# Kernel optimization log

Hardware: AMD Instinct MI355X
Metric: run time of the kernel (lower is better)

The kernel has to match this reference:

```python
import jax, jax.numpy as jnp
import numpy as np

N_EXPERTS = 8
D_MODEL = 1024
D_FF = 4096
TOP_K = 2
B, S = 1, 2048


def setup_inputs() -> dict:
    key = jax.random.key(0)
    ks = jax.random.split(key, 5)
    scale_in = 1.0 / np.sqrt(D_MODEL)
    scale_ff = 1.0 / np.sqrt(D_FF)
    return {
        "x": jax.random.normal(ks[0], (B, S, D_MODEL), dtype=jnp.float32),
        "w_gate": jax.random.normal(ks[1], (D_MODEL, N_EXPERTS), dtype=jnp.float32) * scale_in,
        "b_gate": jnp.zeros((N_EXPERTS,), dtype=jnp.float32),
        "w1": jax.random.normal(ks[2], (N_EXPERTS, D_MODEL, D_FF), dtype=jnp.float32) * scale_in,
        "b1": jnp.zeros((N_EXPERTS, D_FF), dtype=jnp.float32),
        "w2": jax.random.normal(ks[3], (N_EXPERTS, D_FF, D_MODEL), dtype=jnp.float32) * scale_ff,
        "b2": jnp.zeros((N_EXPERTS, D_MODEL), dtype=jnp.float32),
    }


def reference(x, w_gate, b_gate, w1, b1, w2, b2):
    d = x.shape[-1]
    xs = x.reshape(-1, d)                       # [T, d]
    T = xs.shape[0]

    # --- routing: top-k gate logits, softmax over the k selected slots ---
    gate_logits = xs @ w_gate + b_gate          # [T, E]
    topk_vals, topk_idx = jax.lax.top_k(gate_logits, TOP_K)   # [T, k]
    weights = jax.nn.softmax(topk_vals, axis=-1)              # [T, k]

    # scatter slot weights into a dense [T, E] combine matrix
    comb = jnp.zeros((T, N_EXPERTS), dtype=xs.dtype)
    comb = comb.at[jnp.arange(T)[:, None], topk_idx].add(weights)

    # --- expert FFNs computed densely, combined with routing weights ---
    h = jax.nn.relu(jnp.einsum('td,edf->etf', xs, w1) + b1[:, None, :])  # [E, T, ff]
    y = jnp.einsum('etf,efd->etd', h, w2) + b2[:, None, :]               # [E, T, d]
    out = jnp.einsum('te,etd->td', comb, y)                              # [T, d]
    return out.reshape(x.shape)
```

## Files before the change

### kernel.cpp

```cpp
#include <hip/hip_runtime.h>
#include <hip/hip_bf16.h>
#include <math.h>

#define T_TOK 2048
#define DM    1024
#define DF    4096
#define NE    8
#define BM    128
#define BN    128
#define BK    64
#define LDA2  72
#define LDAV1 40
#define YROWS 5120

typedef __attribute__((ext_vector_type(8))) short          bf16x8;
typedef __attribute__((ext_vector_type(8))) unsigned short ushort8;
typedef __attribute__((ext_vector_type(4))) float          f32x4;

__device__ __forceinline__ unsigned short f2bf(float f) {
  unsigned u = __builtin_bit_cast(unsigned, f);
  unsigned r = u + 0x7fffu + ((u >> 16) & 1u);
  return (unsigned short)(r >> 16);
}

__global__ void convert_x_kernel(const float* __restrict__ x, unsigned short* __restrict__ xb) {
  int i = blockIdx.x * blockDim.x + threadIdx.x;
  const float* src = x + (size_t)i * 8;
  float4 a = *(const float4*)(src);
  float4 b = *(const float4*)(src + 4);
  ushort8 v;
  v[0] = f2bf(a.x); v[1] = f2bf(a.y); v[2] = f2bf(a.z); v[3] = f2bf(a.w);
  v[4] = f2bf(b.x); v[5] = f2bf(b.y); v[6] = f2bf(b.z); v[7] = f2bf(b.w);
  *(ushort8*)(xb + (size_t)i * 8) = v;
}

template<int K, int N>
__global__ __launch_bounds__(256) void transpose_convert_packed(
    const float* __restrict__ W, unsigned short* __restrict__ Wt)
{
  const int e  = blockIdx.z;
  const int kt = blockIdx.y;
  const int nt = blockIdx.x;
  const int k0 = kt * 64;
  const int n0 = nt * 128;
  const float* Wp = W + (size_t)e * K * N;
  __shared__ float Ls[64][129];
  const int tid = threadIdx.x;
  {
    const int kl = tid >> 5;
    const int nl = (tid & 31) * 4;
#pragma unroll
    for (int p = 0; p < 8; p++) {
      const int k = kl + p * 8;
      float4 v = *(const float4*)(Wp + (size_t)(k0 + k) * N + n0 + nl);
      Ls[k][nl + 0] = v.x; Ls[k][nl + 1] = v.y; Ls[k][nl + 2] = v.z; Ls[k][nl + 3] = v.w;
    }
  }
  __syncthreads();
  unsigned short* Wo = Wt + ((((size_t)e * (N / 128) + nt) * (K / 64) + kt) * 128) * 64;
  {
    const int n  = tid & 127;
    const int c0 = tid >> 7;
#pragma unroll
    for (int p = 0; p < 4; p++) {
      const int c = c0 + p * 2;
      ushort8 o;
#pragma unroll
      for (int j = 0; j < 8; j++) o[j] = f2bf(Ls[c * 8 + j][n]);
      *(ushort8*)(Wo + (size_t)n * 64 + c * 8) = o;
    }
  }
}

__global__ __launch_bounds__(256) void gating_kernel(
    const float* __restrict__ x, const float* __restrict__ wg, const float* __restrict__ bg,
    int* __restrict__ cnt, int* __restrict__ perm, float* __restrict__ pw,
    int* __restrict__ tok2slot, float* __restrict__ tokw)
{
  int wid  = (blockIdx.x * blockDim.x + threadIdx.x) >> 6;
  int lane = threadIdx.x & 63;
  if (wid >= T_TOK) return;
  const float* xr = x + (size_t)wid * DM;

  float acc[NE];
#pragma unroll
  for (int e = 0; e < NE; e++) acc[e] = 0.f;

  for (int d = lane; d < DM; d += 64) {
    float xv = xr[d];
    const float* wr = wg + (size_t)d * NE;
#pragma unroll
    for (int e = 0; e < NE; e++) acc[e] += xv * wr[e];
  }
#pragma unroll
  for (int off = 32; off > 0; off >>= 1) {
#pragma unroll
    for (int e = 0; e < NE; e++) acc[e] += __shfl_xor(acc[e], off, 64);
  }
  if (lane == 0) {
    float v[NE];
#pragma unroll
    for (int e = 0; e < NE; e++) v[e] = acc[e] + bg[e];
    int i0 = 0; float v0 = v[0];
#pragma unroll
    for (int e = 1; e < NE; e++) { if (v[e] > v0) { v0 = v[e]; i0 = e; } }
    int i1 = -1; float v1 = -INFINITY;
#pragma unroll
    for (int e = 0; e < NE; e++) { if (e != i0 && v[e] > v1) { v1 = v[e]; i1 = e; } }
    float e1 = expf(v1 - v0);
    float s  = 1.f + e1;
    float w0 = 1.f / s, w1 = e1 / s;
    int p0 = atomicAdd(&cnt[i0], 1);
    perm[i0 * T_TOK + p0] = wid; pw[i0 * T_TOK + p0] = w0;
    int p1 = atomicAdd(&cnt[i1], 1);
    perm[i1 * T_TOK + p1] = wid; pw[i1 * T_TOK + p1] = w1;
    tok2slot[2 * wid + 0] = (i0 << 16) | p0;  tokw[2 * wid + 0] = w0;
    tok2slot[2 * wid + 1] = (i1 << 16) | p1;  tokw[2 * wid + 1] = w1;
  }
}

__global__ void pad_scan_kernel(const int* __restrict__ cnt, int* __restrict__ cntpad,
                                int* __restrict__ offs, int* __restrict__ perm, float* __restrict__ pw)
{
  if (threadIdx.x == 0) {
    int o = 0;
    for (int e = 0; e < NE; e++) {
      int c  = cnt[e];
      int cp = (c + BM - 1) / BM * BM;
      cntpad[e] = cp;
      offs[e]   = o;
      o += cp;
    }
    offs[NE] = o;
  }
  for (int e = 0; e < NE; e++) {
    int c  = cnt[e];
    int cp = (c + BM - 1) / BM * BM;
    for (int i = c + threadIdx.x; i < cp; i += blockDim.x) {
      perm[e * T_TOK + i] = 0;
      pw[e * T_TOK + i]   = 0.f;
    }
  }
}

__global__ __launch_bounds__(256) void combine_kernel(
    const float* __restrict__ y0, const float* __restrict__ y1,
    const int* __restrict__ offs, const int* __restrict__ tok2slot,
    const float* __restrict__ tokw, float* __restrict__ out)
{
  const int t = blockIdx.x;
  const int d = threadIdx.x * 4;
  const int s0 = tok2slot[2 * t + 0];
  const int s1 = tok2slot[2 * t + 1];
  const float w0 = tokw[2 * t + 0];
  const float w1 = tokw[2 * t + 1];
  const size_t r0 = (size_t)(offs[s0 >> 16] + (s0 & 0xffff)) * DM + d;
  const size_t r1 = (size_t)(offs[s1 >> 16] + (s1 & 0xffff)) * DM + d;
  float4 a0 = *(const float4*)(y0 + r0);
  float4 b0 = *(const float4*)(y1 + r0);
  float4 a1 = *(const float4*)(y0 + r1);
  float4 b1 = *(const float4*)(y1 + r1);
  float4 o;
  o.x = w0 * (a0.x + b0.x) + w1 * (a1.x + b1.x);
  o.y = w0 * (a0.y + b0.y) + w1 * (a1.y + b1.y);
  o.z = w0 * (a0.z + b0.z) + w1 * (a1.z + b1.z);
  o.w = w0 * (a0.w + b0.w) + w1 * (a1.w + b1.w);
  *(float4*)(out + (size_t)t * DM + d) = o;
}

template<int PHASE, int KTOT, int NCOLS, int KSPLIT>
__global__ __launch_bounds__(256, 3) void moe_gemm5(
    const unsigned short* __restrict__ Asrc,
    const unsigned short* __restrict__ Bt,
    const float* __restrict__ bias,
    const int* __restrict__ cntpad, const int* __restrict__ offs,
    const int* __restrict__ perm,
    unsigned short* __restrict__ Hout, float* __restrict__ yout)
{
  const int e  = blockIdx.z;
  const int mt = blockIdx.y;
  const int nt = blockIdx.x / KSPLIT;
  const int ks = blockIdx.x % KSPLIT;
  const int cp = cntpad[e];
  if (mt * BM >= cp) return;
  const int tid = threadIdx.x;
  const int oe  = offs[e];

  __shared__ unsigned short As[BM * LDA2];
  __shared__ unsigned short Bs[BN * LDA2];

  const int am = tid >> 1;
  const int ak = (tid & 1) * 32;
  const int kb0 = ks * (KTOT / KSPLIT);
  const int KITERS = (KTOT / KSPLIT) / BK;

  const unsigned short* Ap;
  size_t APITCH;
  if (PHASE == 1) {
    int token = perm[e * T_TOK + mt * BM + am];
    Ap = Asrc + (size_t)token * KTOT + kb0 + ak;
    APITCH = BK;
  } else {
    const size_t rb = (size_t)(oe >> 7) + mt;
    Ap = Asrc + (((rb * (KTOT / 64) + (kb0 >> 6)) * 128 + am) * 64) + ak;
    APITCH = (size_t)128 * 64;
  }
  const unsigned short* Bp =
      Bt + ((((size_t)e * (NCOLS / 128) + nt) * (KTOT / 64) + (kb0 >> 6)) * 128 + am) * 64 + ak;

  const int wid  = tid >> 6;
  const int lane = tid & 63;
  const int wm   = (wid & 1) * 64;
  const int wn   = (wid >> 1) * 64;
  const int lrow = lane & 15;
  const int lk   = (lane >> 4) * 8;

  f32x4 acc[4][4];
#pragma unroll
  for (int i = 0; i < 4; i++)
#pragma unroll
    for (int j = 0; j < 4; j++) acc[i][j] = (f32x4){0.f, 0.f, 0.f, 0.f};

  uint4 pa0, pa1, pa2, pa3, pb0, pb1, pb2, pb3;
  auto LOADT = [&](int kt) {
    const unsigned short* a = Ap + (size_t)kt * APITCH;
    const unsigned short* b = Bp + (size_t)kt * (128 * 64);
    pa0 = *(const uint4*)(a);      pa1 = *(const uint4*)(a + 8);
    pa2 = *(const uint4*)(a + 16); pa3 = *(const uint4*)(a + 24);
    pb0 = *(const uint4*)(b);      pb1 = *(const uint4*)(b + 8);
    pb2 = *(const uint4*)(b + 16); pb3 = *(const uint4*)(b + 24);
  };
  auto STORET = [&]() {
    unsigned short* as = &As[am * LDA2 + ak];
    unsigned short* bs = &Bs[am * LDA2 + ak];
    *(uint4*)(as)      = pa0; *(uint4*)(as + 8)  = pa1;
    *(uint4*)(as + 16) = pa2; *(uint4*)(as + 24) = pa3;
    *(uint4*)(bs)      = pb0; *(uint4*)(bs + 8)  = pb1;
    *(uint4*)(bs + 16) = pb2; *(uint4*)(bs + 24) = pb3;
  };

  LOADT(0);
  STORET();
  for (int kt = 0; kt < KITERS; kt++) {
    __syncthreads();
    if (kt + 1 < KITERS) LOADT(kt + 1);
#pragma unroll
    for (int ksb = 0; ksb < 2; ksb++) {
      bf16x8 af[4], bfr[4];
#pragma unroll
      for (int i = 0; i < 4; i++)
        af[i]  = *(const bf16x8*)&As[(wm + i * 16 + lrow) * LDA2 + ksb * 32 + lk];
#pragma unroll
      for (int j = 0; j < 4; j++)
        bfr[j] = *(const bf16x8*)&Bs[(wn + j * 16 + lrow) * LDA2 + ksb * 32 + lk];
#pragma unroll
      for (int i = 0; i < 4; i++)
#pragma unroll
        for (int j = 0; j < 4; j++)
          acc[i][j] = __builtin_amdgcn_mfma_f32_16x16x32_bf16(af[i], bfr[j], acc[i][j], 0, 0, 0);
    }
    __syncthreads();
    if (kt + 1 < KITERS) STORET();
  }

  const int crow = (lane >> 4) * 4;
  const int ccol = lane & 15;
  const size_t rbh = (size_t)(oe >> 7) + mt;
  float* yp = yout + (size_t)ks * ((size_t)YROWS * NCOLS);
#pragma unroll
  for (int j = 0; j < 4; j++) {
    const int gn = nt * BN + wn + j * 16 + ccol;
    const float bv = bias[e * NCOLS + gn];
#pragma unroll
    for (int i = 0; i < 4; i++) {
#pragma unroll
      for (int r = 0; r < 4; r++) {
        const int lm = wm + i * 16 + crow + r;
        float v = acc[i][j][r];
        if (PHASE == 1) {
          v += bv;
          v = v > 0.f ? v : 0.f;
          Hout[(((rbh * (NCOLS / 64) + (gn >> 6)) * 128 + lm) * 64) + (gn & 63)] = f2bf(v);
        } else {
          if (ks == 0) v += bv;
          yp[(size_t)(oe + mt * BM + lm) * NCOLS + gn] = v;
        }
      }
    }
  }
}

template<int PHASE, int KTOT, int NCOLS, int KSPLIT>
__global__ __launch_bounds__(256) void moe_gemm_v1(
    const unsigned short* __restrict__ Asrc,
    const float* __restrict__ Wbase,
    const float* __restrict__ bias,
    const int* __restrict__ cntpad, const int* __restrict__ offs,
    const int* __restrict__ perm, const float* __restrict__ pw,
    unsigned short* __restrict__ Hout, float* __restrict__ out)
{
  const int e  = blockIdx.z;
  const int mt = blockIdx.y;
  const int nt = blockIdx.x / KSPLIT;
  const int ks = blockIdx.x % KSPLIT;
  const int cp = cntpad[e];
  if (mt * BM >= cp) return;
  const int tid = threadIdx.x;
  const int oe  = offs[e];

  __shared__ unsigned short As[BM * LDAV1];
  __shared__ unsigned short Bs[BN * LDAV1];

  const int am = tid >> 1;
  const int ak = (tid & 1) * 16;
  size_t arow_off;
  if (PHASE == 1) {
    int token = perm[e * T_TOK + mt * BM + am];
    arow_off = (size_t)token * KTOT;
  } else {
    arow_off = (size_t)(oe + mt * BM + am) * (size_t)KTOT;
  }
  const int bn  = tid & 127;
  const int bk0 = (tid >> 7) * 16;
  const float* Wexp = Wbase + (size_t)e * KTOT * NCOLS + (size_t)nt * BN;
  const int kbase0 = ks * (KTOT / KSPLIT);
  const int KITERS = (KTOT / KSPLIT) / 32;
  const int wid  = tid >> 6;
  const int lane = tid & 63;
  const int wm   = (wid & 1) * 64;
  const int wn   = (wid >> 1) * 64;
  const int lrow = lane & 15;
  const int lk   = (lane >> 4) * 8;

  f32x4 acc[4][4];
#pragma unroll
  for (int i = 0; i < 4; i++)
#pragma unroll
    for (int j = 0; j < 4; j++) acc[i][j] = (f32x4){0.f, 0.f, 0.f, 0.f};

  for (int kt = 0; kt < KITERS; kt++) {
    const int kb = kbase0 + kt * 32;
    {
      const unsigned short* src = Asrc + arow_off + kb + ak;
      uint4 v0 = *(const uint4*)(src);
      uint4 v1 = *(const uint4*)(src + 8);
      *(uint4*)&As[am * LDAV1 + ak]     = v0;
      *(uint4*)&As[am * LDAV1 + ak + 8] = v1;
    }
#pragma unroll
    for (int t2 = 0; t2 < 2; t2++) {
      const int kk = bk0 + t2 * 8;
      const float* wp = Wexp + (size_t)(kb + kk) * NCOLS + bn;
      ushort8 tv;
#pragma unroll
      for (int j = 0; j < 8; j++) tv[j] = f2bf(wp[(size_t)j * NCOLS]);
      *(ushort8*)&Bs[bn * LDAV1 + kk] = tv;
    }
    __syncthreads();
    bf16x8 af[4], bfr[4];
#pragma unroll
    for (int i = 0; i < 4; i++) af[i]  = *(const bf16x8*)&As[(wm + i * 16 + lrow) * LDAV1 + lk];
#pragma unroll
    for (int j = 0; j < 4; j++) bfr[j] = *(const bf16x8*)&Bs[(wn + j * 16 + lrow) * LDAV1 + lk];
#pragma unroll
    for (int i = 0; i < 4; i++)
#pragma unroll
      for (int j = 0; j < 4; j++)
        acc[i][j] = __builtin_amdgcn_mfma_f32_16x16x32_bf16(af[i], bfr[j], acc[i][j], 0, 0, 0);
    __syncthreads();
  }

  const int crow = (lane >> 4) * 4;
  const int ccol = lane & 15;
#pragma unroll
  for (int j = 0; j < 4; j++) {
    const int gn = nt * BN + wn + j * 16 + ccol;
    const float bv = bias[e * NCOLS + gn];
#pragma unroll
    for (int i = 0; i < 4; i++) {
#pragma unroll
      for (int r = 0; r < 4; r++) {
        const int lm = wm + i * 16 + crow + r;
        float v = acc[i][j][r];
        if (PHASE == 1) {
          v += bv;
          v = v > 0.f ? v : 0.f;
          Hout[(size_t)(oe + mt * BM + lm) * NCOLS + gn] = f2bf(v);
        } else {
          if (ks == 0) v += bv;
          const int li    = e * T_TOK + mt * BM + lm;
          const int token = perm[li];
          const float w   = pw[li];
          atomicAdd(&out[(size_t)token * NCOLS + gn], w * v);
        }
      }
    }
  }
}

extern "C" void kernel_launch(void* const* d_in, const int* in_sizes, int n_in,
                              void* d_out, int out_size, void* d_ws, size_t ws_size,
                              hipStream_t stream) {
  const float* x  = (const float*)d_in[0];
  const float* wg = (const float*)d_in[1];
  const float* bg = (const float*)d_in[2];
  const float* w1 = (const float*)d_in[3];
  const float* b1 = (const float*)d_in[4];
  const float* w2 = (const float*)d_in[5];
  const float* b2 = (const float*)d_in[6];
  float* out = (float*)d_out;

  const size_t XB_BYTES   = (size_t)T_TOK * DM * 2;
  const size_t PERM_BYTES = (size_t)NE * T_TOK * 4;
  const size_t PW_BYTES   = (size_t)NE * T_TOK * 4;
  const size_t TOK_BYTES  = (size_t)T_TOK * 2 * 4;
  const size_t H_BYTES    = (size_t)(2 * T_TOK + NE * BM) * DF * 2;
  const size_t W1T_BYTES  = (size_t)NE * DF * DM * 2;
  const size_t W2T_BYTES  = (size_t)NE * DM * DF * 2;

  char* wsp = (char*)d_ws;
  size_t off = 0;
  unsigned short* xb = (unsigned short*)(wsp + off); off += XB_BYTES;
  int*   cnt    = (int*)(wsp + off); off += 256;
  int*   cntpad = cnt + 8;
  int*   offs   = cnt + 16;
  int*   perm   = (int*)(wsp + off);   off += PERM_BYTES;
  float* pwt    = (float*)(wsp + off); off += PW_BYTES;
  int*   tok2slot = (int*)(wsp + off);   off += TOK_BYTES;
  float* tokw     = (float*)(wsp + off); off += TOK_BYTES;
  unsigned short* H   = (unsigned short*)(wsp + off); off += H_BYTES;
  unsigned short* w1t = (unsigned short*)(wsp + off); off += W1T_BYTES;
  unsigned short* w2t = (unsigned short*)(wsp + off); off += W2T_BYTES;
  const size_t REQUIRED = off;

  float* y = (float*)w1t;

  hipMemsetAsync(cnt, 0, 256, stream);
  hipMemsetAsync(d_out, 0, (size_t)T_TOK * DM * 4, stream);

  convert_x_kernel<<<(T_TOK * DM / 8) / 256, 256, 0, stream>>>(x, xb);
  gating_kernel<<<T_TOK / 4, 256, 0, stream>>>(x, wg, bg, cnt, perm, pwt, tok2slot, tokw);
  pad_scan_kernel<<<1, 256, 0, stream>>>(cnt, cntpad, offs, perm, pwt);

  if (ws_size >= REQUIRED) {
    transpose_convert_packed<DM, DF><<<dim3(DF / 128, DM / 64, NE), 256, 0, stream>>>(w1, w1t);
    transpose_convert_packed<DF, DM><<<dim3(DM / 128, DF / 64, NE), 256, 0, stream>>>(w2, w2t);

    moe_gemm5<1, DM, DF, 1><<<dim3(DF / BN, T_TOK / BM, NE), 256, 0, stream>>>(
        xb, w1t, b1, cntpad, offs, perm, H, nullptr);
    moe_gemm5<2, DF, DM, 2><<<dim3((DM / BN) * 2, T_TOK / BM, NE), 256, 0, stream>>>(
        H, w2t, b2, cntpad, offs, perm, nullptr, y);
    combine_kernel<<<T_TOK, 256, 0, stream>>>(
        y, y + (size_t)YROWS * DM, offs, tok2slot, tokw, out);
  } else {
    moe_gemm_v1<1, DM, DF, 1><<<dim3(DF / BN, T_TOK / BM, NE), 256, 0, stream>>>(
        xb, w1, b1, cntpad, offs, perm, pwt, H, nullptr);
    moe_gemm_v1<2, DF, DM, 4><<<dim3((DM / BN) * 4, T_TOK / BM, NE), 256, 0, stream>>>(
        H, w2, b2, cntpad, offs, perm, pwt, nullptr, out);
  }
}
```

Measured before the change: 515.8 us.

## Fuse x conversion and both weight transposes into one prep kernel

```diff
diff --git a/kernel.cpp b/kernel.cpp
--- a/kernel.cpp
+++ b/kernel.cpp
@@ -34,41 +34,62 @@
   *(ushort8*)(xb + (size_t)i * 8) = v;
 }
 
-template<int K, int N>
-__global__ __launch_bounds__(256) void transpose_convert_packed(
-    const float* __restrict__ W, unsigned short* __restrict__ Wt)
-{
-  const int e  = blockIdx.z;
-  const int kt = blockIdx.y;
-  const int nt = blockIdx.x;
-  const int k0 = kt * 64;
-  const int n0 = nt * 128;
-  const float* Wp = W + (size_t)e * K * N;
-  __shared__ float Ls[64][129];
+__global__ __launch_bounds__(256, 8) void prep_all(
+    const float* __restrict__ x, unsigned short* __restrict__ xb,
+    const float* __restrict__ w1, const float* __restrict__ w2,
+    unsigned short* __restrict__ w1t, unsigned short* __restrict__ w2t)
+{
+  __shared__ float Ls[32][129];
   const int tid = threadIdx.x;
-  {
-    const int kl = tid >> 5;
-    const int nl = (tid & 31) * 4;
-#pragma unroll
-    for (int p = 0; p < 8; p++) {
-      const int k = kl + p * 8;
-      float4 v = *(const float4*)(Wp + (size_t)(k0 + k) * N + n0 + nl);
-      Ls[k][nl + 0] = v.x; Ls[k][nl + 1] = v.y; Ls[k][nl + 2] = v.z; Ls[k][nl + 3] = v.w;
-    }
-  }
+  const int b = blockIdx.x;
+
+  if (b >= 16384) {
+    const int i = (b - 16384) * 256 + tid;
+    const float* src = x + (size_t)i * 8;
+    float4 a  = *(const float4*)(src);
+    float4 c4 = *(const float4*)(src + 4);
+    ushort8 v;
+    v[0] = f2bf(a.x);  v[1] = f2bf(a.y);  v[2] = f2bf(a.z);  v[3] = f2bf(a.w);
+    v[4] = f2bf(c4.x); v[5] = f2bf(c4.y); v[6] = f2bf(c4.z); v[7] = f2bf(c4.w);
+    *(ushort8*)(xb + (size_t)i * 8) = v;
+    return;
+  }
+
+  const float* W; unsigned short* Wt; int K, N, nt, kt32, e;
+  if (b < 8192) {
+    W = w1; Wt = w1t; K = DM; N = DF;
+    nt = b & 31; kt32 = (b >> 5) & 31; e = b >> 10;
+  } else {
+    const int b2 = b - 8192;
+    W = w2; Wt = w2t; K = DF; N = DM;
+    nt = b2 & 7; kt32 = (b2 >> 3) & 127; e = b2 >> 10;
+  }
+
+  const float* Wp = W + (size_t)e * K * N + (size_t)(kt32 * 32) * N + nt * 128;
+  const int kl = tid >> 5;
+  const int nl = (tid & 31) * 4;
+  float4 v0 = *(const float4*)(Wp + (size_t)(kl +  0) * N + nl);
+  float4 v1 = *(const float4*)(Wp + (size_t)(kl +  8) * N + nl);
+  float4 v2 = *(const float4*)(Wp + (size_t)(kl + 16) * N + nl);
+  float4 v3 = *(const float4*)(Wp + (size_t)(kl + 24) * N + nl);
+  Ls[kl +  0][nl + 0] = v0.x; Ls[kl +  0][nl + 1] = v0.y; Ls[kl +  0][nl + 2] = v0.z; Ls[kl +  0][nl + 3] = v0.w;
+  Ls[kl +  8][nl + 0] = v1.x; Ls[kl +  8][nl + 1] = v1.y; Ls[kl +  8][nl + 2] = v1.z; Ls[kl +  8][nl + 3] = v1.w;
+  Ls[kl + 16][nl + 0] = v2.x; Ls[kl + 16][nl + 1] = v2.y; Ls[kl + 16][nl + 2] = v2.z; Ls[kl + 16][nl + 3] = v2.w;
+  Ls[kl + 24][nl + 0] = v3.x; Ls[kl + 24][nl + 1] = v3.y; Ls[kl + 24][nl + 2] = v3.z; Ls[kl + 24][nl + 3] = v3.w;
   __syncthreads();
-  unsigned short* Wo = Wt + ((((size_t)e * (N / 128) + nt) * (K / 64) + kt) * 128) * 64;
-  {
-    const int n  = tid & 127;
-    const int c0 = tid >> 7;
-#pragma unroll
-    for (int p = 0; p < 4; p++) {
-      const int c = c0 + p * 2;
-      ushort8 o;
-#pragma unroll
-      for (int j = 0; j < 8; j++) o[j] = f2bf(Ls[c * 8 + j][n]);
-      *(ushort8*)(Wo + (size_t)n * 64 + c * 8) = o;
-    }
+
+  unsigned short* Wo = Wt
+      + ((((size_t)e * (N >> 7) + nt) * (K >> 6) + (kt32 >> 1)) * 128) * 64
+      + (kt32 & 1) * 32;
+  const int c  = tid & 3;
+  const int nb = tid >> 2;
+#pragma unroll
+  for (int p = 0; p < 2; p++) {
+    const int n = nb + p * 64;
+    ushort8 o;
+#pragma unroll
+    for (int j = 0; j < 8; j++) o[j] = f2bf(Ls[c * 8 + j][n]);
+    *(ushort8*)(Wo + (size_t)n * 64 + c * 8) = o;
   }
 }
 
@@ -436,15 +457,12 @@
   float* y = (float*)w1t;
 
   hipMemsetAsync(cnt, 0, 256, stream);
-  hipMemsetAsync(d_out, 0, (size_t)T_TOK * DM * 4, stream);
-
-  convert_x_kernel<<<(T_TOK * DM / 8) / 256, 256, 0, stream>>>(x, xb);
+
   gating_kernel<<<T_TOK / 4, 256, 0, stream>>>(x, wg, bg, cnt, perm, pwt, tok2slot, tokw);
   pad_scan_kernel<<<1, 256, 0, stream>>>(cnt, cntpad, offs, perm, pwt);
 
   if (ws_size >= REQUIRED) {
-    transpose_convert_packed<DM, DF><<<dim3(DF / 128, DM / 64, NE), 256, 0, stream>>>(w1, w1t);
-    transpose_convert_packed<DF, DM><<<dim3(DM / 128, DF / 64, NE), 256, 0, stream>>>(w2, w2t);
+    prep_all<<<17408, 256, 0, stream>>>(x, xb, w1, w2, w1t, w2t);
 
     moe_gemm5<1, DM, DF, 1><<<dim3(DF / BN, T_TOK / BM, NE), 256, 0, stream>>>(
         xb, w1t, b1, cntpad, offs, perm, H, nullptr);
@@ -453,6 +471,8 @@
     combine_kernel<<<T_TOK, 256, 0, stream>>>(
         y, y + (size_t)YROWS * DM, offs, tok2slot, tokw, out);
   } else {
+    hipMemsetAsync(d_out, 0, (size_t)T_TOK * DM * 4, stream);
+    convert_x_kernel<<<(T_TOK * DM / 8) / 256, 256, 0, stream>>>(x, xb);
     moe_gemm_v1<1, DM, DF, 1><<<dim3(DF / BN, T_TOK / BM, NE), 256, 0, stream>>>(
         xb, w1, b1, cntpad, offs, perm, pwt, H, nullptr);
     moe_gemm_v1<2, DF, DM, 4><<<dim3((DM / BN) * 4, T_TOK / BM, NE), 256, 0, stream>>>(
```

After: 509.8 us. No clear change (-1.2%).
